# Kernel optimization log

Hardware: AMD Instinct MI355X
Metric: run time of the kernel (lower is better)

The kernel has to match this reference:

```python
import jax, jax.numpy as jnp
import numpy as np

ANCHOR_PX = (32, 64, 96, 128)
FIELD = 16.0
POOL, TILES = 2, 3
TAU, NMS_IOU = 0.5, 0.3
MAX_DET = 512
HF, WF, DF = 128, 128, 512
HIDDEN = 1024


def _create_anchors():
    # anchors centered on the field grid, rows ordered (i, j, k): x,y = upper-left, w=h=size
    ii, jj, kk = np.meshgrid(np.arange(HF), np.arange(WF), np.arange(len(ANCHOR_PX)), indexing='ij')
    sz = np.asarray(ANCHOR_PX, np.float32)[kk]
    x = jj * FIELD + FIELD / 2 - sz / 2
    y = ii * FIELD + FIELD / 2 - sz / 2
    return np.stack([x.ravel(), y.ravel(), sz.ravel(), sz.ravel()], axis=1).astype(np.float32)


def setup_inputs() -> dict:
    key = jax.random.key(0)
    ks = jax.random.split(key, 8)
    return {
        'features': jax.random.normal(ks[0], (HF, WF, DF), jnp.float32),
        'rpn_obj': jax.random.normal(ks[1], (HF, WF, 2 * len(ANCHOR_PX)), jnp.float32),
        'rpn_reg': 0.1 * jax.random.normal(ks[2], (HF, WF, 4 * len(ANCHOR_PX)), jnp.float32),
        'anchors': jnp.asarray(_create_anchors()),
        'W1': 0.02 * jax.random.normal(ks[3], (TILES * TILES * DF, HIDDEN), jnp.float32),
        'b1': jnp.zeros((HIDDEN,), jnp.float32),
        'W2': 0.02 * jax.random.normal(ks[4], (HIDDEN, HIDDEN), jnp.float32),
        'b2': jnp.zeros((HIDDEN,), jnp.float32),
        'W3': 0.02 * jax.random.normal(ks[5], (HIDDEN, 4), jnp.float32),
        'b3': jnp.zeros((4,), jnp.float32),
    }


def _map_outputs(output, anchors):
    # faithful port of map_outputs: 3D RPN tensor -> per-anchor rows via gather
    K = len(ANCHOR_PX)
    ap = jnp.asarray(ANCHOR_PX, jnp.float32)
    idx = jnp.argmax(anchors[:, 3:4] == ap[None, :], axis=1).astype(jnp.int32)
    px = ((anchors[:, 0] + anchors[:, 2] / 2) / FIELD).astype(jnp.int32)
    py = ((anchors[:, 1] + anchors[:, 3] / 2) / FIELD).astype(jnp.int32)
    H, W, D = output.shape
    reshaped = output.reshape(H, W, K, D // K)
    return reshaped[py, px, idx]  # (Na, D//K)


def _unparameterize(reg, anchors):
    acx = anchors[:, 0] + anchors[:, 2] / 2
    acy = anchors[:, 1] + anchors[:, 3] / 2
    cx = acx + reg[:, 0] * anchors[:, 2]
    cy = acy + reg[:, 1] * anchors[:, 3]
    w = anchors[:, 2] * jnp.exp(reg[:, 2])
    h = anchors[:, 3] * jnp.exp(reg[:, 3])
    return jnp.stack([cx - w / 2, cy - h / 2, w, h], axis=1)


def _iou_matrix(boxes):
    x1, y1 = boxes[:, 0], boxes[:, 1]
    x2, y2 = x1 + boxes[:, 2], y1 + boxes[:, 3]
    ix = jnp.maximum(0.0, jnp.minimum(x2[:, None], x2[None, :]) - jnp.maximum(x1[:, None], x1[None, :]))
    iy = jnp.maximum(0.0, jnp.minimum(y2[:, None], y2[None, :]) - jnp.maximum(y1[:, None], y1[None, :]))
    inter = ix * iy
    area = boxes[:, 2] * boxes[:, 3]
    return inter / (area[:, None] + area[None, :] - inter + 1e-8)


def _nms_keep(iou, valid, thr):
    # greedy NMS on score-sorted boxes: sequential scan over rows
    n = valid.shape[0]
    rng = jnp.arange(n)
    def step(keep, i):
        suppressed = jnp.any((iou[i] > thr) & keep & (rng < i))
        k = valid[i] & jnp.logical_not(suppressed)
        return keep.at[i].set(k), k
    keep, _ = jax.lax.scan(step, jnp.zeros((n,), bool), rng)
    return keep


def _roialign(features, boxes):
    # pool x pool bilinear samples per tile, tiles x tiles tiles per box, max-pooled per tile
    M = boxes.shape[0]
    T = TILES * POOL
    t = (jnp.arange(T, dtype=jnp.float32) + 0.5) / T
    fx = (boxes[:, 0:1] + t[None, :] * boxes[:, 2:3]) / FIELD - 0.5  # (M, T)
    fy = (boxes[:, 1:2] + t[None, :] * boxes[:, 3:4]) / FIELD - 0.5
    def grid(c, n):
        c = jnp.clip(c, 0.0, n - 1.0)
        c0 = jnp.floor(c).astype(jnp.int32)
        c1 = jnp.minimum(c0 + 1, n - 1)
        return c0, c1, c - c0
    x0, x1, wx = grid(fx, WF)
    y0, y1, wy = grid(fy, HF)
    def g(yi, xi):
        return features[yi[:, :, None], xi[:, None, :]]  # (M, T, T, D)
    wy0, wy1 = (1 - wy)[:, :, None, None], wy[:, :, None, None]
    wx0, wx1 = (1 - wx)[:, None, :, None], wx[:, None, :, None]
    val = g(y0, x0) * wy0 * wx0 + g(y0, x1) * wy0 * wx1 + g(y1, x0) * wy1 * wx0 + g(y1, x1) * wy1 * wx1
    val = val.reshape(M, TILES, POOL, TILES, POOL, DF)
    return jnp.max(val, axis=(2, 4))  # (M, TILES, TILES, D)


def reference(features, rpn_obj, rpn_reg, anchors, W1, b1, W2, b2, W3, b3):
    obj = _map_outputs(rpn_obj, anchors)            # (Na, 2)
    reg = _map_outputs(rpn_reg, anchors)            # (Na, 4)
    scores = jax.nn.softmax(obj, axis=1)[:, 1]      # objectness
    boxes = _unparameterize(reg, anchors)           # proposals (Na, 4)
    # threshold + top-k (fixed-shape surrogate for boolean_mask)
    masked = jnp.where(scores > TAU, scores, -jnp.inf)
    top_scores, top_idx = jax.lax.top_k(masked, MAX_DET)
    valid = jnp.isfinite(top_scores)
    sel = boxes[top_idx]                            # (MAX_DET, 4)
    keep = _nms_keep(_iou_matrix(sel), valid, NMS_IOU)
    # roialign + fast-rcnn refinement head
    pooled = _roialign(features, sel).reshape(MAX_DET, -1)
    h = jax.nn.relu(pooled @ W1 + b1)
    h = jax.nn.relu(h @ W2 + b2)
    deltas = h @ W3 + b3
    refined = _unparameterize(deltas, sel)
    sc = jnp.where(valid, top_scores, 0.0)
    out = jnp.concatenate([refined, sc[:, None]], axis=1)
    return out * keep[:, None].astype(out.dtype)    # (MAX_DET, 5)
```

## Files before the change

kernel.cpp:

```cpp
#include <hip/hip_runtime.h>
#include <math.h>

#define HFD 128
#define WFD 128
#define DFD 512
#define KA  4
#define NA  (HFD*WFD*KA)
#define MAXD 512
#define HID 1024
#define FIN 4608
#define CMAX 2048
#define NBUCK 1025
#define BINCAP 64
#define TAUF 0.5f
#define NMS_THR 0.3f
#define SPLITK 8

typedef __bf16 bf16x8 __attribute__((ext_vector_type(8)));
typedef float  floatx4 __attribute__((ext_vector_type(4)));

__device__ __forceinline__ unsigned short f2bf(float x) {
    unsigned u = __float_as_uint(x);
    unsigned r = (u + 0x7FFFu + ((u >> 16) & 1u)) >> 16;
    return (unsigned short)r;
}

__global__ void init_kernel(unsigned* __restrict__ hist) {
    int t = threadIdx.x;
    for (int i = t; i < NBUCK; i += 1024) hist[i] = 0u;
}

__global__ __launch_bounds__(256)
void front_kernel(const float* __restrict__ rpn_obj,
                  unsigned* __restrict__ hist,
                  unsigned long long* __restrict__ bins,
                  const float* __restrict__ W1,
                  unsigned short* __restrict__ W1t,
                  const float* __restrict__ W2,
                  unsigned short* __restrict__ W2t) {
    __shared__ float tile[32][33];
    int b = blockIdx.x;
    if (b < 256) {
        int n = b * 256 + threadIdx.x;
        float2 o = ((const float2*)rpn_obj)[n];
        float m  = fmaxf(o.x, o.y);
        float e0 = expf(o.x - m), e1 = expf(o.y - m);
        float s  = e1 / (e0 + e1);
        if (s > TAUF) {
            unsigned bits = __float_as_uint(s);
            unsigned bk = (bits - 0x3F000000u) >> 13;
            unsigned slot = atomicAdd(&hist[bk], 1u);
            if (slot < BINCAP)
                bins[bk * BINCAP + slot] =
                    ((unsigned long long)bits << 32) |
                    (unsigned long long)(~(unsigned)n);
        }
        return;
    }
    b -= 256;
    const float* W; unsigned short* Wt; int K, N;
    if (b < (FIN / 32) * (HID / 32)) { W = W1; Wt = W1t; K = FIN; N = HID; }
    else { b -= (FIN / 32) * (HID / 32); W = W2; Wt = W2t; K = HID; N = HID; }
    int bn = (b & (N / 32 - 1)) * 32;
    int bk = (b / (N / 32)) * 32;
    int tx = threadIdx.x & 31, ty = threadIdx.x >> 5;
#pragma unroll
    for (int r = 0; r < 32; r += 8)
        tile[ty + r][tx] = W[(long)(bk + ty + r) * N + bn + tx];
    __syncthreads();
#pragma unroll
    for (int r = 0; r < 32; r += 8)
        Wt[(long)(bn + ty + r) * K + bk + tx] = f2bf(tile[tx][ty + r]);
}

__global__ __launch_bounds__(1024)
void tgs_kernel(const unsigned* __restrict__ hist,
                const unsigned long long* __restrict__ bins,
                const float* __restrict__ rpn_reg,
                const float* __restrict__ anchors,
                float* __restrict__ sel,
                float* __restrict__ top_score,
                unsigned* __restrict__ valid_g) {
    __shared__ unsigned long long keys[CMAX];
    __shared__ unsigned Hs[NBUCK];
    __shared__ unsigned Ssc[1024];
    __shared__ unsigned cntS;
    __shared__ unsigned thrS;

    int tid = threadIdx.x;
    int wave = tid >> 6, lane = tid & 63;

    if (tid == 0) cntS = 0u;
    for (int i = tid; i < NBUCK; i += 1024) Hs[i] = hist[i];
    __syncthreads();
    unsigned sv = Hs[tid + 1];
    Ssc[tid] = sv;
    __syncthreads();
    for (int d = 1; d < 1024; d <<= 1) {
        unsigned add = (tid + d < 1024) ? Ssc[tid + d] : 0u;
        __syncthreads();
        Ssc[tid] += add;
        __syncthreads();
    }
    if (tid == 0 && Ssc[0] < MAXD) thrS = 0u;
    {
        unsigned Scur = Ssc[tid];
        unsigned Snxt = (tid == 1023) ? 0u : Ssc[tid + 1];
        if (Scur >= MAXD && Snxt < MAXD) thrS = (unsigned)(tid + 1);
    }
    __syncthreads();
    unsigned thr = thrS;

    for (int b = (int)thr + wave; b < NBUCK; b += 16) {
        unsigned c = Hs[b]; if (c > BINCAP) c = BINCAP;
        unsigned base = 0;
        if (lane == 0 && c > 0) base = atomicAdd(&cntS, c);
        base = __shfl(base, 0);
        if (c > 0 && lane < c && base + lane < CMAX)
            keys[base + lane] = bins[(long)b * BINCAP + lane];
    }
    __syncthreads();
    unsigned cnt = cntS; if (cnt > CMAX) cnt = CMAX;
    int SN = (cnt <= 1024) ? 1024 : CMAX;
    for (int i = tid; i < SN; i += 1024)
        if (i >= (int)cnt) keys[i] = 0ULL;
    __syncthreads();

    for (int k = 2; k <= SN; k <<= 1) {
        for (int j = k >> 1; j > 0; j >>= 1) {
            for (int i = tid; i < SN; i += 1024) {
                int ixj = i ^ j;
                if (ixj > i) {
                    unsigned long long a = keys[i], b = keys[ixj];
                    bool up = ((i & k) == 0);
                    if ((a < b) == up) { keys[i] = b; keys[ixj] = a; }
                }
            }
            __syncthreads();
        }
    }

    if (tid < MAXD) {
        unsigned long long e = keys[tid];
        unsigned sbits = (unsigned)(e >> 32);
        bool v = (sbits != 0u);
        unsigned idx = v ? (unsigned)(~(unsigned)e) : 0u;
        int cell = idx >> 2, kk = idx & 3;
        float4 rg = *(const float4*)&rpn_reg[cell * 16 + 4 * kk];
        float4 an = *(const float4*)&anchors[idx * 4];
        float acx = an.x + an.z * 0.5f;
        float acy = an.y + an.w * 0.5f;
        float cx = acx + rg.x * an.z;
        float cy = acy + rg.y * an.w;
        float w  = an.z * expf(rg.z);
        float h  = an.w * expf(rg.w);
        ((float4*)sel)[tid] = make_float4(cx - 0.5f * w, cy - 0.5f * h, w, h);
        top_score[tid] = v ? __uint_as_float(sbits) : 0.0f;
        valid_g[tid]   = v ? 1u : 0u;
    }
}

__global__ __launch_bounds__(512)
void iou_mask_kernel(const float* __restrict__ sel,
                     unsigned long long* __restrict__ mask) {
    int i = blockIdx.x;
    int j = threadIdx.x;
    float4 bi = ((const float4*)sel)[i];
    float4 bj = ((const float4*)sel)[j];
    float x2i = bi.x + bi.z, y2i = bi.y + bi.w;
    float x2j = bj.x + bj.z, y2j = bj.y + bj.w;
    float ai = bi.z * bi.w, aj = bj.z * bj.w;
    float ix = fmaxf(0.0f, fminf(x2i, x2j) - fmaxf(bi.x, bj.x));
    float iy = fmaxf(0.0f, fminf(y2i, y2j) - fmaxf(bi.y, bj.y));
    float inter = ix * iy;
    float iou = inter / (ai + aj - inter + 1e-8f);
    unsigned long long bal = __ballot(iou > NMS_THR);
    if ((j & 63) == 0) mask[i * 8 + (j >> 6)] = bal;
}

__global__ __launch_bounds__(64)
void nms_scan_kernel(const unsigned long long* __restrict__ mask,
                     const unsigned* __restrict__ valid,
                     unsigned* __restrict__ keep) {
    int lane = threadIdx.x;
    unsigned long long w[8][8];
#pragma unroll
    for (int g = 0; g < 8; ++g)
#pragma unroll
        for (int t = 0; t < 8; ++t)
            if (t <= g) w[g][t] = mask[(g * 64 + lane) * 8 + t];
    unsigned long long vb[8];
#pragma unroll
    for (int g = 0; g < 8; ++g)
        vb[g] = __ballot(valid[g * 64 + lane] != 0u);

    unsigned long long keepw[8];
#pragma unroll
    for (int g = 0; g < 8; ++g) {
        bool pre = false;
#pragma unroll
        for (int t = 0; t < 8; ++t)
            if (t < g) pre = pre || ((w[g][t] & keepw[t]) != 0ULL);
        unsigned long long alive = vb[g] & ~__ballot(pre);
        unsigned long long intra = w[g][g];
        unsigned long long kg = 0ULL;
        while (alive) {
            int b = __builtin_ctzll(alive);
            unsigned long long bit = 1ULL << b;
            kg |= bit;
            unsigned long long sup = __ballot((intra >> b) & 1ULL);
            alive &= ~(sup | bit);
        }
        keepw[g] = kg;
        keep[g * 64 + lane] = (unsigned)((kg >> lane) & 1ULL);
    }
}

__global__ __launch_bounds__(256)
void roialign_kernel(const float* __restrict__ feat,
                     const float* __restrict__ sel,
                     unsigned short* __restrict__ pooled) {
    int mrow = blockIdx.x;
    int c = threadIdx.x;
    float4 b = ((const float4*)sel)[mrow];
    float bx = b.x, by = b.y, bw = b.z, bh = b.w;
    float vmax0[9], vmax1[9];
#pragma unroll
    for (int t = 0; t < 9; ++t) { vmax0[t] = -INFINITY; vmax1[t] = -INFINITY; }
#pragma unroll
    for (int p = 0; p < 6; ++p) {
        float fy = (by + ((float)p + 0.5f) / 6.0f * bh) / 16.0f - 0.5f;
        fy = fminf(fmaxf(fy, 0.0f), 127.0f);
        int y0 = (int)floorf(fy);
        int y1 = min(y0 + 1, 127);
        float wy = fy - (float)y0;
#pragma unroll
        for (int q = 0; q < 6; ++q) {
            float fx = (bx + ((float)q + 0.5f) / 6.0f * bw) / 16.0f - 0.5f;
            fx = fminf(fmaxf(fx, 0.0f), 127.0f);
            int x0 = (int)floorf(fx);
            int x1 = min(x0 + 1, 127);
            float wx = fx - (float)x0;
            const float* f00 = feat + (y0 * WFD + x0) * DFD;
            const float* f01 = feat + (y0 * WFD + x1) * DFD;
            const float* f10 = feat + (y1 * WFD + x0) * DFD;
            const float* f11 = feat + (y1 * WFD + x1) * DFD;
            float w00 = (1.0f - wy) * (1.0f - wx);
            float w01 = (1.0f - wy) * wx;
            float w10 = wy * (1.0f - wx);
            float w11 = wy * wx;
            int t = (p >> 1) * 3 + (q >> 1);
            float v0 = f00[c] * w00 + f01[c] * w01 + f10[c] * w10 + f11[c] * w11;
            float v1 = f00[c + 256] * w00 + f01[c + 256] * w01 +
                       f10[c + 256] * w10 + f11[c + 256] * w11;
            vmax0[t] = fmaxf(vmax0[t], v0);
            vmax1[t] = fmaxf(vmax1[t], v1);
        }
    }
#pragma unroll
    for (int t = 0; t < 9; ++t) {
        pooled[mrow * FIN + t * DFD + c] = f2bf(vmax0[t]);
        pooled[mrow * FIN + t * DFD + c + 256] = f2bf(vmax1[t]);
    }
}

#define LDSTRIDE 40
__global__ __launch_bounds__(256)
void mfma_gemm_kernel(const unsigned short* __restrict__ A,
                      const unsigned short* __restrict__ Bt,
                      float* __restrict__ Cpart,
                      int M, int N, int K) {
    __shared__ unsigned short As[64 * LDSTRIDE];
    __shared__ unsigned short Bs[64 * LDSTRIDE];
    int tid = threadIdx.x;
    int wave = tid >> 6, lane = tid & 63;
    int bm = blockIdx.y * 64, bn = blockIdx.x * 64;
    int KC = K / SPLITK;
    int ks = blockIdx.z * KC;

    floatx4 acc[4] = {};
    int lr = tid >> 2;
    int lk = (tid & 3) << 3;
    int frow = lane & 15, quad = lane >> 4;

    const unsigned short* Ap = A + (long)(bm + lr) * K + lk;
    const unsigned short* Bp = Bt + (long)(bn + lr) * K + lk;

    for (int k0 = ks; k0 < ks + KC; k0 += 32) {
        uint4 av = *(const uint4*)(Ap + k0);
        uint4 bv = *(const uint4*)(Bp + k0);
        *(uint4*)&As[lr * LDSTRIDE + lk] = av;
        *(uint4*)&Bs[lr * LDSTRIDE + lk] = bv;
        __syncthreads();
        bf16x8 af = *(const bf16x8*)&As[(wave * 16 + frow) * LDSTRIDE + quad * 8];
#pragma unroll
        for (int t = 0; t < 4; ++t) {
            bf16x8 bfv = *(const bf16x8*)&Bs[(t * 16 + frow) * LDSTRIDE + quad * 8];
            acc[t] = __builtin_amdgcn_mfma_f32_16x16x32_bf16(af, bfv, acc[t], 0, 0, 0);
        }
        __syncthreads();
    }

    float* Cp = Cpart + (long)blockIdx.z * M * N;
#pragma unroll
    for (int t = 0; t < 4; ++t) {
#pragma unroll
        for (int r = 0; r < 4; ++r) {
            int m = bm + wave * 16 + quad * 4 + r;
            int n = bn + t * 16 + frow;
            Cp[(long)m * N + n] = acc[t][r];
        }
    }
}

__global__ __launch_bounds__(256)
void reduce_bias_relu_kernel(const float* __restrict__ Cpart,
                             const float* __restrict__ bias,
                             unsigned short* __restrict__ out_bf,
                             int MN, int N) {
    int i4 = (blockIdx.x * blockDim.x + threadIdx.x) * 4;
    if (i4 >= MN) return;
    float4 s = *(const float4*)&Cpart[i4];
#pragma unroll
    for (int z = 1; z < SPLITK; ++z) {
        float4 p = *(const float4*)&Cpart[(long)z * MN + i4];
        s.x += p.x; s.y += p.y; s.z += p.z; s.w += p.w;
    }
    int n = i4 & (N - 1);
    float4 bi = *(const float4*)&bias[n];
    s.x = fmaxf(s.x + bi.x, 0.0f);
    s.y = fmaxf(s.y + bi.y, 0.0f);
    s.z = fmaxf(s.z + bi.z, 0.0f);
    s.w = fmaxf(s.w + bi.w, 0.0f);
    uint2 o;
    o.x = (unsigned)f2bf(s.x) | ((unsigned)f2bf(s.y) << 16);
    o.y = (unsigned)f2bf(s.z) | ((unsigned)f2bf(s.w) << 16);
    *(uint2*)&out_bf[i4] = o;
}

__global__ __launch_bounds__(256)
void rowhead_kernel(const float* __restrict__ Cpart,
                    const float* __restrict__ b2,
                    const float* __restrict__ W3,
                    const float* __restrict__ b3,
                    const float* __restrict__ sel,
                    const float* __restrict__ top_score,
                    const unsigned* __restrict__ valid,
                    const unsigned* __restrict__ keep,
                    float* __restrict__ out) {
    __shared__ float red[4][4];
    int r = blockIdx.x, t = threadIdx.x;
    int wave = t >> 6, lane = t & 63;
    int c = t * 4;
    const int MN = MAXD * HID;
    float4 s = *(const float4*)&Cpart[(long)r * HID + c];
#pragma unroll
    for (int z = 1; z < SPLITK; ++z) {
        float4 p = *(const float4*)&Cpart[(long)z * MN + (long)r * HID + c];
        s.x += p.x; s.y += p.y; s.z += p.z; s.w += p.w;
    }
    float4 bi = *(const float4*)&b2[c];
    float h[4];
    h[0] = fmaxf(s.x + bi.x, 0.0f);
    h[1] = fmaxf(s.y + bi.y, 0.0f);
    h[2] = fmaxf(s.z + bi.z, 0.0f);
    h[3] = fmaxf(s.w + bi.w, 0.0f);
    float a0 = 0.f, a1 = 0.f, a2 = 0.f, a3 = 0.f;
#pragma unroll
    for (int i = 0; i < 4; ++i) {
        float4 w = *(const float4*)&W3[(c + i) * 4];
        a0 += h[i] * w.x; a1 += h[i] * w.y;
        a2 += h[i] * w.z; a3 += h[i] * w.w;
    }
#pragma unroll
    for (int off = 32; off > 0; off >>= 1) {
        a0 += __shfl_down(a0, off);
        a1 += __shfl_down(a1, off);
        a2 += __shfl_down(a2, off);
        a3 += __shfl_down(a3, off);
    }
    if (lane == 0) {
        red[wave][0] = a0; red[wave][1] = a1;
        red[wave][2] = a2; red[wave][3] = a3;
    }
    __syncthreads();
    if (t == 0) {
        float d0 = red[0][0] + red[1][0] + red[2][0] + red[3][0] + b3[0];
        float d1 = red[0][1] + red[1][1] + red[2][1] + red[3][1] + b3[1];
        float d2 = red[0][2] + red[1][2] + red[2][2] + red[3][2] + b3[2];
        float d3 = red[0][3] + red[1][3] + red[2][3] + red[3][3] + b3[3];
        if (keep[r] != 0u) {
            float4 b = ((const float4*)sel)[r];
            float acx = b.x + 0.5f * b.z;
            float acy = b.y + 0.5f * b.w;
            float cx = acx + d0 * b.z;
            float cy = acy + d1 * b.w;
            float nw = b.z * expf(d2);
            float nh = b.w * expf(d3);
            out[r * 5 + 0] = cx - 0.5f * nw;
            out[r * 5 + 1] = cy - 0.5f * nh;
            out[r * 5 + 2] = nw;
            out[r * 5 + 3] = nh;
            out[r * 5 + 4] = (valid[r] != 0u) ? top_score[r] : 0.0f;
        } else {
            out[r * 5 + 0] = 0.0f;
            out[r * 5 + 1] = 0.0f;
            out[r * 5 + 2] = 0.0f;
            out[r * 5 + 3] = 0.0f;
            out[r * 5 + 4] = 0.0f;
        }
    }
}

extern "C" void kernel_launch(void* const* d_in, const int* in_sizes, int n_in,
                              void* d_out, int out_size, void* d_ws, size_t ws_size,
                              hipStream_t stream) {
    const float* features = (const float*)d_in[0];
    const float* rpn_obj  = (const float*)d_in[1];
    const float* rpn_reg  = (const float*)d_in[2];
    const float* anchors  = (const float*)d_in[3];
    const float* W1 = (const float*)d_in[4];
    const float* b1 = (const float*)d_in[5];
    const float* W2 = (const float*)d_in[6];
    const float* b2 = (const float*)d_in[7];
    const float* W3 = (const float*)d_in[8];
    const float* b3 = (const float*)d_in[9];
    float* out = (float*)d_out;

    char* ws = (char*)d_ws;
    size_t off = 0;
    auto alloc = [&](size_t bytes) {
        char* p = ws + off;
        off += (bytes + 255) & ~(size_t)255;
        return p;
    };
    unsigned* hist      = (unsigned*)alloc(NBUCK * sizeof(unsigned));
    unsigned long long* bins =
        (unsigned long long*)alloc((size_t)NBUCK * BINCAP * 8);
    float*    sel       = (float*)alloc(MAXD * 4 * sizeof(float));
    float*    top_score = (float*)alloc(MAXD * sizeof(float));
    unsigned* valid     = (unsigned*)alloc(MAXD * sizeof(unsigned));
    unsigned* keep      = (unsigned*)alloc(MAXD * sizeof(unsigned));
    unsigned long long* mask = (unsigned long long*)alloc(MAXD * 8 * 8);
    unsigned short* pooled = (unsigned short*)alloc((size_t)MAXD * FIN * 2);
    unsigned short* W1t = (unsigned short*)alloc((size_t)FIN * HID * 2);
    unsigned short* W2t = (unsigned short*)alloc((size_t)HID * HID * 2);
    unsigned short* h1  = (unsigned short*)alloc((size_t)MAXD * HID * 2);
    float*    Cpart     = (float*)alloc((size_t)SPLITK * MAXD * HID * sizeof(float));
    (void)ws_size; (void)in_sizes; (void)n_in; (void)out_size;

    const int TBLOCKS = (FIN / 32) * (HID / 32) + (HID / 32) * (HID / 32);
    init_kernel<<<1, 1024, 0, stream>>>(hist);
    front_kernel<<<256 + TBLOCKS, 256, 0, stream>>>(rpn_obj, hist, bins,
                                                    W1, W1t, W2, W2t);
    tgs_kernel<<<1, 1024, 0, stream>>>(hist, bins, rpn_reg, anchors,
                                       sel, top_score, valid);
    iou_mask_kernel<<<MAXD, 512, 0, stream>>>(sel, mask);
    nms_scan_kernel<<<1, 64, 0, stream>>>(mask, valid, keep);
    roialign_kernel<<<MAXD, 256, 0, stream>>>(features, sel, pooled);

    const int MN = MAXD * HID;
    mfma_gemm_kernel<<<dim3(HID / 64, MAXD / 64, SPLITK), 256, 0, stream>>>(
        pooled, W1t, Cpart, MAXD, HID, FIN);
    reduce_bias_relu_kernel<<<MN / 4 / 256, 256, 0, stream>>>(
        Cpart, b1, h1, MN, HID);
    mfma_gemm_kernel<<<dim3(HID / 64, MAXD / 64, SPLITK), 256, 0, stream>>>(
        h1, W2t, Cpart, MAXD, HID, HID);
    rowhead_kernel<<<MAXD, 256, 0, stream>>>(Cpart, b2, W3, b3, sel,
                                             top_score, valid, keep, out);
}
```

Baseline: 203.6 us.

## Compact NMS survivors and drop split-K in favour of fused bias-ReLU GEMM epilogues

The NMS scan now emits a compacted list of kept box indices and a count, so RoIAlign, both GEMMs and the head run only on surviving rows; output rows for suppressed boxes are zeroed with a memset. The split-K GEMM and its separate reduce kernels are removed: each GEMM block now loops over the full K and applies bias and ReLU in its epilogue. This also drops the large partial-sum buffer traffic. A memset replaces the histogram init kernel. The trade-off is far fewer GEMM blocks (128 rather than 1024) with long serial K loops, which can leave most compute units idle.

```diff
diff --git a/kernel.cpp b/kernel.cpp
--- a/kernel.cpp
+++ b/kernel.cpp
@@ -14,7 +14,6 @@
 #define BINCAP 64
 #define TAUF 0.5f
 #define NMS_THR 0.3f
-#define SPLITK 8
 
 typedef __bf16 bf16x8 __attribute__((ext_vector_type(8)));
 typedef float  floatx4 __attribute__((ext_vector_type(4)));
@@ -23,11 +22,6 @@
     unsigned u = __float_as_uint(x);
     unsigned r = (u + 0x7FFFu + ((u >> 16) & 1u)) >> 16;
     return (unsigned short)r;
-}
-
-__global__ void init_kernel(unsigned* __restrict__ hist) {
-    int t = threadIdx.x;
-    for (int i = t; i < NBUCK; i += 1024) hist[i] = 0u;
 }
 
 __global__ __launch_bounds__(256)
@@ -181,7 +175,8 @@
 __global__ __launch_bounds__(64)
 void nms_scan_kernel(const unsigned long long* __restrict__ mask,
                      const unsigned* __restrict__ valid,
-                     unsigned* __restrict__ keep) {
+                     unsigned* __restrict__ cidx,
+                     unsigned* __restrict__ nkeep) {
     int lane = threadIdx.x;
     unsigned long long w[8][8];
 #pragma unroll
@@ -212,15 +207,30 @@
             alive &= ~(sup | bit);
         }
         keepw[g] = kg;
-        keep[g * 64 + lane] = (unsigned)((kg >> lane) & 1ULL);
-    }
+    }
+    unsigned total = 0;
+#pragma unroll
+    for (int g = 0; g < 8; ++g) {
+        unsigned long long kg = keepw[g];
+        if ((kg >> lane) & 1ULL) {
+            unsigned pos = total +
+                (unsigned)__builtin_popcountll(kg & ((1ULL << lane) - 1ULL));
+            cidx[pos] = (unsigned)(g * 64 + lane);
+        }
+        total += (unsigned)__builtin_popcountll(kg);
+    }
+    if (lane == 0) nkeep[0] = total;
 }
 
 __global__ __launch_bounds__(256)
 void roialign_kernel(const float* __restrict__ feat,
                      const float* __restrict__ sel,
+                     const unsigned* __restrict__ cidx,
+                     const unsigned* __restrict__ nkeep,
                      unsigned short* __restrict__ pooled) {
-    int mrow = blockIdx.x;
+    int m = blockIdx.x;
+    if (m >= (int)nkeep[0]) return;
+    int mrow = (int)cidx[m];
     int c = threadIdx.x;
     float4 b = ((const float4*)sel)[mrow];
     float bx = b.x, by = b.y, bw = b.z, bh = b.w;
@@ -259,24 +269,27 @@
     }
 #pragma unroll
     for (int t = 0; t < 9; ++t) {
-        pooled[mrow * FIN + t * DFD + c] = f2bf(vmax0[t]);
-        pooled[mrow * FIN + t * DFD + c + 256] = f2bf(vmax1[t]);
+        pooled[m * FIN + t * DFD + c] = f2bf(vmax0[t]);
+        pooled[m * FIN + t * DFD + c + 256] = f2bf(vmax1[t]);
     }
 }
 
 #define LDSTRIDE 40
 __global__ __launch_bounds__(256)
-void mfma_gemm_kernel(const unsigned short* __restrict__ A,
-                      const unsigned short* __restrict__ Bt,
-                      float* __restrict__ Cpart,
-                      int M, int N, int K) {
+void gemm_fused_kernel(const unsigned short* __restrict__ A,
+                       const unsigned short* __restrict__ Bt,
+                       const float* __restrict__ bias,
+                       unsigned short* __restrict__ out_bf,
+                       float* __restrict__ out_f,
+                       const unsigned* __restrict__ nkeep,
+                       int N, int K) {
+    int bm = blockIdx.y * 64;
+    if (bm >= (int)nkeep[0]) return;
     __shared__ unsigned short As[64 * LDSTRIDE];
     __shared__ unsigned short Bs[64 * LDSTRIDE];
     int tid = threadIdx.x;
     int wave = tid >> 6, lane = tid & 63;
-    int bm = blockIdx.y * 64, bn = blockIdx.x * 64;
-    int KC = K / SPLITK;
-    int ks = blockIdx.z * KC;
+    int bn = blockIdx.x * 64;
 
     floatx4 acc[4] = {};
     int lr = tid >> 2;
@@ -286,7 +299,7 @@
     const unsigned short* Ap = A + (long)(bm + lr) * K + lk;
     const unsigned short* Bp = Bt + (long)(bn + lr) * K + lk;
 
-    for (int k0 = ks; k0 < ks + KC; k0 += 32) {
+    for (int k0 = 0; k0 < K; k0 += 32) {
         uint4 av = *(const uint4*)(Ap + k0);
         uint4 bv = *(const uint4*)(Bp + k0);
         *(uint4*)&As[lr * LDSTRIDE + lk] = av;
@@ -301,70 +314,37 @@
         __syncthreads();
     }
 
-    float* Cp = Cpart + (long)blockIdx.z * M * N;
 #pragma unroll
     for (int t = 0; t < 4; ++t) {
+        int n = bn + t * 16 + frow;
+        float bv = bias[n];
 #pragma unroll
         for (int r = 0; r < 4; ++r) {
             int m = bm + wave * 16 + quad * 4 + r;
-            int n = bn + t * 16 + frow;
-            Cp[(long)m * N + n] = acc[t][r];
+            float v = fmaxf(acc[t][r] + bv, 0.0f);
+            if (out_bf) out_bf[(long)m * N + n] = f2bf(v);
+            else        out_f[(long)m * N + n]  = v;
         }
     }
 }
 
 __global__ __launch_bounds__(256)
-void reduce_bias_relu_kernel(const float* __restrict__ Cpart,
-                             const float* __restrict__ bias,
-                             unsigned short* __restrict__ out_bf,
-                             int MN, int N) {
-    int i4 = (blockIdx.x * blockDim.x + threadIdx.x) * 4;
-    if (i4 >= MN) return;
-    float4 s = *(const float4*)&Cpart[i4];
-#pragma unroll
-    for (int z = 1; z < SPLITK; ++z) {
-        float4 p = *(const float4*)&Cpart[(long)z * MN + i4];
-        s.x += p.x; s.y += p.y; s.z += p.z; s.w += p.w;
-    }
-    int n = i4 & (N - 1);
-    float4 bi = *(const float4*)&bias[n];
-    s.x = fmaxf(s.x + bi.x, 0.0f);
-    s.y = fmaxf(s.y + bi.y, 0.0f);
-    s.z = fmaxf(s.z + bi.z, 0.0f);
-    s.w = fmaxf(s.w + bi.w, 0.0f);
-    uint2 o;
-    o.x = (unsigned)f2bf(s.x) | ((unsigned)f2bf(s.y) << 16);
-    o.y = (unsigned)f2bf(s.z) | ((unsigned)f2bf(s.w) << 16);
-    *(uint2*)&out_bf[i4] = o;
-}
-
-__global__ __launch_bounds__(256)
-void rowhead_kernel(const float* __restrict__ Cpart,
-                    const float* __restrict__ b2,
+void rowhead_kernel(const float* __restrict__ h2,
                     const float* __restrict__ W3,
                     const float* __restrict__ b3,
                     const float* __restrict__ sel,
                     const float* __restrict__ top_score,
-                    const unsigned* __restrict__ valid,
-                    const unsigned* __restrict__ keep,
+                    const unsigned* __restrict__ cidx,
+                    const unsigned* __restrict__ nkeep,
                     float* __restrict__ out) {
+    int p = blockIdx.x;
+    if (p >= (int)nkeep[0]) return;
     __shared__ float red[4][4];
-    int r = blockIdx.x, t = threadIdx.x;
+    int t = threadIdx.x;
     int wave = t >> 6, lane = t & 63;
     int c = t * 4;
-    const int MN = MAXD * HID;
-    float4 s = *(const float4*)&Cpart[(long)r * HID + c];
-#pragma unroll
-    for (int z = 1; z < SPLITK; ++z) {
-        float4 p = *(const float4*)&Cpart[(long)z * MN + (long)r * HID + c];
-        s.x += p.x; s.y += p.y; s.z += p.z; s.w += p.w;
-    }
-    float4 bi = *(const float4*)&b2[c];
-    float h[4];
-    h[0] = fmaxf(s.x + bi.x, 0.0f);
-    h[1] = fmaxf(s.y + bi.y, 0.0f);
-    h[2] = fmaxf(s.z + bi.z, 0.0f);
-    h[3] = fmaxf(s.w + bi.w, 0.0f);
+    float4 s = *(const float4*)&h2[(long)p * HID + c];
+    float h[4] = {s.x, s.y, s.z, s.w};
     float a0 = 0.f, a1 = 0.f, a2 = 0.f, a3 = 0.f;
 #pragma unroll
     for (int i = 0; i < 4; ++i) {
@@ -385,30 +365,23 @@
     }
     __syncthreads();
     if (t == 0) {
+        int r = (int)cidx[p];
         float d0 = red[0][0] + red[1][0] + red[2][0] + red[3][0] + b3[0];
         float d1 = red[0][1] + red[1][1] + red[2][1] + red[3][1] + b3[1];
         float d2 = red[0][2] + red[1][2] + red[2][2] + red[3][2] + b3[2];
         float d3 = red[0][3] + red[1][3] + red[2][3] + red[3][3] + b3[3];
-        if (keep[r] != 0u) {
-            float4 b = ((const float4*)sel)[r];
-            float acx = b.x + 0.5f * b.z;
-            float acy = b.y + 0.5f * b.w;
-            float cx = acx + d0 * b.z;
-            float cy = acy + d1 * b.w;
-            float nw = b.z * expf(d2);
-            float nh = b.w * expf(d3);
-            out[r * 5 + 0] = cx - 0.5f * nw;
-            out[r * 5 + 1] = cy - 0.5f * nh;
-            out[r * 5 + 2] = nw;
-            out[r * 5 + 3] = nh;
-            out[r * 5 + 4] = (valid[r] != 0u) ? top_score[r] : 0.0f;
-        } else {
-            out[r * 5 + 0] = 0.0f;
-            out[r * 5 + 1] = 0.0f;
-            out[r * 5 + 2] = 0.0f;
-            out[r * 5 + 3] = 0.0f;
-            out[r * 5 + 4] = 0.0f;
-        }
+        float4 b = ((const float4*)sel)[r];
+        float acx = b.x + 0.5f * b.z;
+        float acy = b.y + 0.5f * b.w;
+        float cx = acx + d0 * b.z;
+        float cy = acy + d1 * b.w;
+        float nw = b.z * expf(d2);
+        float nh = b.w * expf(d3);
+        out[r * 5 + 0] = cx - 0.5f * nw;
+        out[r * 5 + 1] = cy - 0.5f * nh;
+        out[r * 5 + 2] = nw;
+        out[r * 5 + 3] = nh;
+        out[r * 5 + 4] = top_score[r];
     }
 }
 
@@ -440,32 +413,32 @@
     float*    sel       = (float*)alloc(MAXD * 4 * sizeof(float));
     float*    top_score = (float*)alloc(MAXD * sizeof(float));
     unsigned* valid     = (unsigned*)alloc(MAXD * sizeof(unsigned));
-    unsigned* keep      = (unsigned*)alloc(MAXD * sizeof(unsigned));
+    unsigned* cidx      = (unsigned*)alloc(MAXD * sizeof(unsigned));
+    unsigned* nkeep     = (unsigned*)alloc(sizeof(unsigned));
     unsigned long long* mask = (unsigned long long*)alloc(MAXD * 8 * 8);
     unsigned short* pooled = (unsigned short*)alloc((size_t)MAXD * FIN * 2);
     unsigned short* W1t = (unsigned short*)alloc((size_t)FIN * HID * 2);
     unsigned short* W2t = (unsigned short*)alloc((size_t)HID * HID * 2);
     unsigned short* h1  = (unsigned short*)alloc((size_t)MAXD * HID * 2);
-    float*    Cpart     = (float*)alloc((size_t)SPLITK * MAXD * HID * sizeof(float));
-    (void)ws_size; (void)in_sizes; (void)n_in; (void)out_size;
+    float*    h2        = (float*)alloc((size_t)MAXD * HID * sizeof(float));
+    (void)ws_size; (void)in_sizes; (void)n_in;
+
+    hipMemsetAsync(hist, 0, NBUCK * sizeof(unsigned), stream);
+    hipMemsetAsync(out, 0, (size_t)out_size * sizeof(float), stream);
 
     const int TBLOCKS = (FIN / 32) * (HID / 32) + (HID / 32) * (HID / 32);
-    init_kernel<<<1, 1024, 0, stream>>>(hist);
     front_kernel<<<256 + TBLOCKS, 256, 0, stream>>>(rpn_obj, hist, bins,
                                                     W1, W1t, W2, W2t);
     tgs_kernel<<<1, 1024, 0, stream>>>(hist, bins, rpn_reg, anchors,
                                        sel, top_score, valid);
     iou_mask_kernel<<<MAXD, 512, 0, stream>>>(sel, mask);
-    nms_scan_kernel<<<1, 64, 0, stream>>>(mask, valid, keep);
-    roialign_kernel<<<MAXD, 256, 0, stream>>>(features, sel, pooled);
-
-    const int MN = MAXD * HID;
-    mfma_gemm_kernel<<<dim3(HID / 64, MAXD / 64, SPLITK), 256, 0, stream>>>(
-        pooled, W1t, Cpart, MAXD, HID, FIN);
-    reduce_bias_relu_kernel<<<MN / 4 / 256, 256, 0, stream>>>(
-        Cpart, b1, h1, MN, HID);
-    mfma_gemm_kernel<<<dim3(HID / 64, MAXD / 64, SPLITK), 256, 0, stream>>>(
-        h1, W2t, Cpart, MAXD, HID, HID);
-    rowhead_kernel<<<MAXD, 256, 0, stream>>>(Cpart, b2, W3, b3, sel,
-                                             top_score, valid, keep, out);
-}
+    nms_scan_kernel<<<1, 64, 0, stream>>>(mask, valid, cidx, nkeep);
+    roialign_kernel<<<MAXD, 256, 0, stream>>>(features, sel, cidx, nkeep,
+                                              pooled);
+    gemm_fused_kernel<<<dim3(HID / 64, MAXD / 64), 256, 0, stream>>>(
+        pooled, W1t, b1, h1, (float*)nullptr, nkeep, HID, FIN);
+    gemm_fused_kernel<<<dim3(HID / 64, MAXD / 64), 256, 0, stream>>>(
+        h1, W2t, b2, (unsigned short*)nullptr, h2, nkeep, HID, HID);
+    rowhead_kernel<<<MAXD, 256, 0, stream>>>(h2, W3, b3, sel, top_score,
+                                             cidx, nkeep, out);
+}
```

New measurement: 245.2 us. +20.5%, slower.
